# Kernel tuning notes

Measured on AMD Instinct MI355X. Metric: run time of the kernel, lower is better.

## Reference

```python
import jax, jax.numpy as jnp
import numpy as np

NUM_HEADS = 8
TEMPERATURE = 10000.0


def sine_embed(pos, dim):
    """Sine positional embedding of 2D offsets. pos [..., 2] -> [..., dim]."""
    half = dim // 2  # dims per coordinate
    dim_t = TEMPERATURE ** (2.0 * (jnp.arange(half) // 2).astype(jnp.float32) / half)
    s = pos[..., :, None] / dim_t  # [..., 2, half]
    emb = jnp.stack([jnp.sin(s[..., 0::2]), jnp.cos(s[..., 1::2])], axis=-1)
    emb = emb.reshape(s.shape[:-1] + (half,))  # interleaved sin/cos per coord
    return emb.reshape(pos.shape[:-1] + (dim,))


def setup_inputs() -> dict:
    key = jax.random.key(0)
    ks = jax.random.split(key, 16)
    N, H, W, C, K = 2, 40, 40, 256, 100
    h = NUM_HEADS
    sc = 1.0 / np.sqrt(C)
    return {
        "query_feature": jax.random.normal(ks[0], (N, H, W, C), jnp.float32),
        "query_position": jax.random.uniform(ks[1], (N, H, W, 2), jnp.float32),
        "key_feature": jax.random.normal(ks[2], (N, K, C), jnp.float32),
        "key_position": jax.random.uniform(ks[3], (N, K, 2), jnp.float32),
        # MultiheadAttention params (torch convention: weight [out, in])
        "in_proj_w": jax.random.normal(ks[4], (3 * C, C), jnp.float32) * sc,
        "in_proj_b": jnp.zeros((3 * C,), jnp.float32),
        "out_proj_w": jax.random.normal(ks[5], (C, C), jnp.float32) * sc,
        "out_proj_b": jnp.zeros((C,), jnp.float32),
        # PositionalEncodingSineLearned MLP: sine(C) -> C -> num_heads
        "pos_w1": jax.random.normal(ks[6], (C, C), jnp.float32) * sc,
        "pos_b1": jnp.zeros((C,), jnp.float32),
        "pos_w2": jax.random.normal(ks[7], (h, C), jnp.float32) * sc,
        "pos_b2": jnp.zeros((h,), jnp.float32),
        # cat_pos branch params
        "pos_trans_w": jax.random.normal(ks[8], (2, 2), jnp.float32),
        "embed_w": jax.random.normal(ks[9], (C, C + 2), jnp.float32) * 0.01,
        "embed_b": jnp.zeros((C,), jnp.float32),
    }


def reference(query_feature, query_position, key_feature, key_position,
              in_proj_w, in_proj_b, out_proj_w, out_proj_b,
              pos_w1, pos_b1, pos_w2, pos_b2,
              pos_trans_w, embed_w, embed_b):
    N, H, W, C = query_feature.shape
    h = NUM_HEADS
    d = C // h
    q = query_feature.reshape(N, -1, C)            # [N,Q,C]
    qp = query_position.reshape(N, -1, 2)          # [N,Q,2] (scale_terms = 1.0)
    Q = q.shape[1]
    K = key_feature.shape[1]

    # pairwise relative positions: [N,Q,K,2]
    rel_pos = key_position[:, None, :, :] - qp[:, :, None, :]

    # learned sine relative positional encoding -> per-head additive bias
    pe = sine_embed(rel_pos, C)                              # [N,Q,K,C]
    hid = jax.nn.relu(pe @ pos_w1.T + pos_b1)                # [N,Q,K,C]
    bias = (hid @ pos_w2.T + pos_b2).transpose(0, 3, 1, 2)   # [N,h,Q,K]

    # multihead attention with additive relative bias
    wq, wk, wv = jnp.split(in_proj_w, 3, axis=0)
    bq, bk, bv = jnp.split(in_proj_b, 3, axis=0)
    qh = ((q @ wq.T + bq).reshape(N, Q, h, d)) * (d ** -0.5)
    kh = (key_feature @ wk.T + bk).reshape(N, K, h, d)
    vh = (key_feature @ wv.T + bv).reshape(N, K, h, d)
    scores = jnp.einsum('nqhd,nkhd->nhqk', qh, kh) + bias
    attn = jax.nn.softmax(scores, axis=-1)                   # [N,h,Q,K]
    ctx = jnp.einsum('nhqk,nkhd->nqhd', attn, vh).reshape(N, Q, C)
    refined = ctx @ out_proj_w.T + out_proj_b                # [N,Q,C]

    # cat_pos: attention-weighted relative position aggregation
    attn_w = attn.mean(axis=1)                               # [N,Q,K]
    new_rel = jnp.einsum('nqk,nqkc->nqc', attn_w, jax.lax.stop_gradient(rel_pos))
    new_pos = new_rel @ pos_trans_w.T                        # [N,Q,2]

    feat = jax.nn.relu(q + refined)
    feat = jax.nn.relu(jnp.concatenate([feat, new_pos], axis=-1) @ embed_w.T + embed_b)
    return feat.reshape(N, H, W, C)
```

## Files before the change

kernel.cpp:

```cpp
#include <hip/hip_runtime.h>
#include <math.h>

typedef __bf16 bf16x8 __attribute__((ext_vector_type(8)));
typedef __bf16 bf16x4 __attribute__((ext_vector_type(4)));
typedef float  f32x4  __attribute__((ext_vector_type(4)));


#define WS_KH    0u
#define WS_VH    51200u
#define WS_EWT   102400u
#define WS_QHB   168960u
#define WS_BIASB 578560u
#define WS_KEB   2012160u
#define WS_W1B   2038560u
#define WS_W2PB  2071328u
#define WS_QEB   2073376u
#define WS_IPWT  2482976u
#define WS_OWT   2679584u

__device__ __forceinline__ float rdlane(float v, int l) {
  return __uint_as_float(__builtin_amdgcn_readlane(__float_as_uint(v), l));
}

__device__ __forceinline__ unsigned packbf(float a, float b) {
  unsigned short ua = __builtin_bit_cast(unsigned short, (__bf16)a);
  unsigned short ub = __builtin_bit_cast(unsigned short, (__bf16)b);
  return (unsigned)ua | ((unsigned)ub << 16);
}

__global__ __launch_bounds__(256, 2) void prep0_kernel(
    const float* __restrict__ ipw, const float* __restrict__ ow,
    const float* __restrict__ ew, float* __restrict__ ws)
{
  __shared__ float tile[64][65];
  int bid = blockIdx.x, t = threadIdx.x;
  int l = t & 63, gq = t >> 6;

  if (bid < 48) {
    int row0 = (bid >> 2) * 64, col0 = (bid & 3) * 64;
#pragma unroll
    for (int i = 0; i < 16; i++) {
      int r = gq * 16 + i;
      tile[r][l] = ipw[(unsigned)(row0 + r) * 256u + col0 + l];
    }
    __syncthreads();
#pragma unroll
    for (int i = 0; i < 16; i++) {
      int r = gq * 16 + i;
      ws[WS_IPWT + (unsigned)(col0 + r) * 768u + row0 + l] = tile[l][r];
    }
  } else if (bid < 64) {
    int b = bid - 48;
    int row0 = (b >> 2) * 64, col0 = (b & 3) * 64;
#pragma unroll
    for (int i = 0; i < 16; i++) {
      int r = gq * 16 + i;
      tile[r][l] = ow[(unsigned)(row0 + r) * 256u + col0 + l];
    }
    __syncthreads();
#pragma unroll
    for (int i = 0; i < 16; i++) {
      int r = gq * 16 + i;
      ws[WS_OWT + (unsigned)(col0 + r) * 256u + row0 + l] = tile[l][r];
    }
  } else {
    int b = bid - 64;
    int row0 = (b / 5) * 64, col0 = (b % 5) * 64;
#pragma unroll
    for (int i = 0; i < 16; i++) {
      int r = gq * 16 + i;
      int cin = col0 + l;
      tile[r][l] = (cin < 258) ? ew[(unsigned)(row0 + r) * 258u + cin] : 0.0f;
    }
    __syncthreads();
#pragma unroll
    for (int i = 0; i < 16; i++) {
      int r = gq * 16 + i;
      int j = col0 + r;
      if (j < 260) ws[WS_EWT + (unsigned)j * 256u + row0 + l] = tile[l][r];
    }
  }
}

__global__ __launch_bounds__(256, 2) void prep_kernel(
    const float* __restrict__ qfeat, const float* __restrict__ kfeat,
    const float* __restrict__ kpos, const float* __restrict__ qpos,
    const float* __restrict__ ipb,
    const float* __restrict__ pos_w1, const float* __restrict__ pos_w2,
    float* __restrict__ ws)
{
  __shared__ float x[8 * 256];
  int bid = blockIdx.x, t = threadIdx.x;

  if (bid < 50) {
    int r = bid * 4 + (t >> 6);
    int u = t & 63;
    float p0 = kpos[r * 2 + 0], p1 = kpos[r * 2 + 1];
    __bf16* keb = (__bf16*)(ws + WS_KEB);
    bf16x4 o;
#pragma unroll
    for (int j = 0; j < 4; j++) {
      int col = u * 4 + j;
      int c = col >> 7, i = (col & 127) >> 1;
      float p = c ? p1 : p0;
      float inv = exp2f((float)i * (-13.287712379549449f / 64.0f));
      float v = p * inv;
      o[j] = (__bf16)((col & 1) ? __cosf(v) : __sinf(v));
    }
    *(bf16x4*)(keb + r * 264 + u * 4) = o;
  } else if (bid < 114) {
    int idx = (bid - 50) * 1024 + t * 4;
    float4 v = *(const float4*)( (const float*)0 == nullptr ? nullptr : nullptr);
    (void)v;
  } else if (bid < 147) {
    return;
  } else if (bid < 547) {
    int r0 = (bid - 147) * 8;
    for (int i = t; i < 2048; i += 256) x[i] = qfeat[(unsigned)r0 * 256u + i];
    __syncthreads();
    float acc[8]; float bq = ipb[t];
#pragma unroll
    for (int rr = 0; rr < 8; rr++) acc[rr] = bq;
    const float* wqt = ws + WS_IPWT + t;
    for (int j = 0; j < 256; j += 4) {
      float w0 = wqt[(unsigned)(j + 0) * 768u];
      float w1 = wqt[(unsigned)(j + 1) * 768u];
      float w2 = wqt[(unsigned)(j + 2) * 768u];
      float w3 = wqt[(unsigned)(j + 3) * 768u];
#pragma unroll
      for (int rr = 0; rr < 8; rr++) {
        float4 x4 = *(const float4*)(x + rr * 256 + j);
        acc[rr] = fmaf(x4.x, w0, fmaf(x4.y, w1, fmaf(x4.z, w2, fmaf(x4.w, w3, acc[rr]))));
      }
    }
    __bf16* qhb = (__bf16*)(ws + WS_QHB);
#pragma unroll
    for (int rr = 0; rr < 8; rr++)
      qhb[(unsigned)(r0 + rr) * 256u + t] = (__bf16)(acc[rr] * 0.17677669529663687f);
  } else if (bid < 579) {
    int b2 = bid - 547; int n = b2 >> 4, tile = b2 & 15;
    int r0l = tile * 7; int cnt = 100 - r0l; if (cnt > 7) cnt = 7; if (cnt <= 0) return;
    int r0 = n * 100 + r0l;
    for (int i = t; i < cnt * 256; i += 256) x[i] = kfeat[(unsigned)r0 * 256u + i];
    __syncthreads();
    float ak[7], av[7]; float bk = ipb[256 + t], bv = ipb[512 + t];
#pragma unroll
    for (int rr = 0; rr < 7; rr++) { ak[rr] = bk; av[rr] = bv; }
    const float* wkt = ws + WS_IPWT + 256 + t;
    const float* wvt = ws + WS_IPWT + 512 + t;
    for (int j = 0; j < 256; j += 2) {
      float k0 = wkt[(unsigned)(j + 0) * 768u];
      float k1 = wkt[(unsigned)(j + 1) * 768u];
      float v0 = wvt[(unsigned)(j + 0) * 768u];
      float v1 = wvt[(unsigned)(j + 1) * 768u];
#pragma unroll
      for (int rr = 0; rr < 7; rr++) {
        float2 x2 = *(const float2*)(x + rr * 256 + j);
        ak[rr] = fmaf(x2.x, k0, fmaf(x2.y, k1, ak[rr]));
        av[rr] = fmaf(x2.x, v0, fmaf(x2.y, v1, av[rr]));
      }
    }
    for (int rr = 0; rr < 7; rr++) {
      if (rr < cnt) {
        ws[WS_KH + (unsigned)(r0 + rr) * 256u + t] = ak[rr];
        ws[WS_VH + (unsigned)(r0 + rr) * 256u + t] = av[rr];
      }
    }
  } else {
    int r = (bid - 579) * 4 + (t >> 6);
    int u = t & 63;
    float p0 = qpos[r * 2 + 0], p1 = qpos[r * 2 + 1];
    __bf16* qeb = (__bf16*)(ws + WS_QEB);
    bf16x4 o;
#pragma unroll
    for (int j = 0; j < 4; j++) {
      int col = u * 4 + j;
      int c = col >> 7, i = (col & 127) >> 1;
      float p = c ? p1 : p0;
      float inv = exp2f((float)i * (-13.287712379549449f / 64.0f));
      float v = p * inv;
      o[j] = (__bf16)((col & 1) ? __cosf(v) : __sinf(v));
    }
    *(bf16x4*)(qeb + r * 256 + u * 4) = o;
  }
}

__global__ __launch_bounds__(256, 2) void prep_w_kernel(
    const float* __restrict__ pos_w1, const float* __restrict__ pos_w2,
    float* __restrict__ ws)
{
  int bid = blockIdx.x, t = threadIdx.x;
  if (bid < 64) {
    int idx = bid * 1024 + t * 4;
    float4 v = *(const float4*)(pos_w1 + idx);
    bf16x4 o; o[0] = (__bf16)v.x; o[1] = (__bf16)v.y; o[2] = (__bf16)v.z; o[3] = (__bf16)v.w;
    *(bf16x4*)((__bf16*)(ws + WS_W1B) + idx) = o;
  } else {
    __bf16* w2pb = (__bf16*)(ws + WS_W2PB);
    for (int i = 0; i < 16; i++) {
      int idx = t * 16 + i;
      w2pb[idx] = (idx < 2048) ? (__bf16)pos_w2[idx] : (__bf16)0.0f;
    }
  }
}

__global__ __launch_bounds__(512, 2) void bias_kernel(
    const float* __restrict__ pos_b1, const float* __restrict__ pos_b2,
    float* __restrict__ ws)
{
  __shared__ __align__(16) char qe_smem[2][32768];
  __shared__ __align__(16) char hid_smem[2][32768];
  __shared__ __align__(16) __bf16 keb_s[256];

  int bid = blockIdx.x;
  int nk = bid / 5, g = bid - nk * 5;
  int n = nk / 100, k = nk - n * 100;
  int qbase = n * 1600 + g * 320;
  int t = threadIdx.x;
  int lane = t & 63, w = t >> 6;
  int wc = w & 3, wq = w >> 2;
  int l15 = lane & 15, quad = lane >> 4;

  const __bf16* keb = (const __bf16*)(ws + WS_KEB) + (unsigned)nk * 264u;
  const __bf16* qeb = (const __bf16*)(ws + WS_QEB);
  const __bf16* w1b = (const __bf16*)(ws + WS_W1B);
  const __bf16* w2pb = (const __bf16*)(ws + WS_W2PB);
  __bf16* biasb = (__bf16*)(ws + WS_BIASB);

  if (t < 32) *(bf16x8*)(keb_s + t * 8) = *(const bf16x8*)(keb + t * 8);

  int sr = t >> 3, ssub = t & 7, sswz = (sr & 7) << 4;
  {
    const __bf16* src = qeb + (unsigned)(qbase + sr) * 256u + ssub * 32;
    char* dst = qe_smem[0] + sr * 512;
#pragma unroll
    for (int u = 0; u < 4; u++) {
      bf16x8 v = *(const bf16x8*)(src + u * 8);
      *(bf16x8*)(dst + ((ssub * 64 + u * 16) ^ sswz)) = v;
    }
  }

  int xm = (l15 & 7) << 4;
  int colx[8];
#pragma unroll
  for (int kc = 0; kc < 8; kc++) colx[kc] = ((kc * 64 + quad * 16) ^ xm);
  const __bf16* w1p = w1b + (unsigned)(wc * 64 + l15) * 256u + quad * 8;

  float b1a[4][4];
#pragma unroll
  for (int ct = 0; ct < 4; ct++)
#pragma unroll
    for (int r = 0; r < 4; r++) b1a[ct][r] = pos_b1[wc * 64 + ct * 16 + quad * 4 + r];
  float b2v[4];
#pragma unroll
  for (int r = 0; r < 4; r++) b2v[r] = pos_b2[(quad * 4 + r) & 7];

  f32x4 zero4; zero4[0] = 0.f; zero4[1] = 0.f; zero4[2] = 0.f; zero4[3] = 0.f;

  __syncthreads();

  bf16x8 af[8][4];
#pragma unroll
  for (int kc = 0; kc < 8; kc++) {
    bf16x8 ke8 = *(const bf16x8*)(keb_s + kc * 32 + quad * 8);
#pragma unroll
    for (int ct = 0; ct < 4; ct++) {
      bf16x8 w8 = *(const bf16x8*)(w1p + ct * 4096 + kc * 32);
      bf16x8 a;
#pragma unroll
      for (int p2 = 0; p2 < 4; p2++) {
        float we = (float)w8[2 * p2], wo = (float)w8[2 * p2 + 1];
        float sk = (float)ke8[2 * p2], ck = (float)ke8[2 * p2 + 1];
        a[2 * p2]     = (__bf16)fmaf(wo, sk, -(we * ck));
        a[2 * p2 + 1] = (__bf16)fmaf(we, sk, wo * ck);
      }
      af[kc][ct] = a;
    }
  }

  unsigned long long bias_pk[5];

  auto gemm2 = [&](int tg) {
    bf16x8 w2f[8];
#pragma unroll
    for (int kc = 0; kc < 8; kc++)
      w2f[kc] = *(const bf16x8*)(w2pb + (unsigned)l15 * 256u + kc * 32 + quad * 8);
    int row = wc * 16 + l15;
    const char* hbase = hid_smem[tg & 1] + row * 512;
    int hxm = (l15 & 7) << 4;
    f32x4 acc2 = zero4;
#pragma unroll
    for (int kc = 0; kc < 8; kc++) {
      bf16x8 hf = *(const bf16x8*)(hbase + ((kc * 64 + quad * 16) ^ hxm));
      acc2 = __builtin_amdgcn_mfma_f32_16x16x32_bf16(w2f[kc], hf, acc2, 0, 0, 0);
    }
    unsigned lo = packbf(acc2[0] + b2v[0], acc2[1] + b2v[1]);
    unsigned hi = packbf(acc2[2] + b2v[2], acc2[3] + b2v[3]);
    return (unsigned long long)lo | ((unsigned long long)hi << 32);
  };

#pragma unroll
  for (int tt = 0; tt < 5; tt++) {
    bf16x8 qv[4];
    if (tt < 4) {
      const __bf16* src = qeb + (unsigned)(qbase + (tt + 1) * 64 + sr) * 256u + ssub * 32;
#pragma unroll
      for (int u = 0; u < 4; u++) qv[u] = *(const bf16x8*)(src + u * 8);
    }

    if (tt > 0 && wq == 0) bias_pk[tt - 1] = gemm2(tt - 1);

    f32x4 acc[4][2];
#pragma unroll
    for (int ct = 0; ct < 4; ct++)
#pragma unroll
      for (int nt = 0; nt < 2; nt++) acc[ct][nt] = zero4;

#pragma unroll
    for (int kc = 0; kc < 8; kc++) {
#pragma unroll
      for (int nt = 0; nt < 2; nt++) {
        int row = wq * 32 + nt * 16 + l15;
        bf16x8 qf = *(const bf16x8*)(qe_smem[tt & 1] + row * 512 + colx[kc]);
        acc[0][nt] = __builtin_amdgcn_mfma_f32_16x16x32_bf16(af[kc][0], qf, acc[0][nt], 0, 0, 0);
        acc[1][nt] = __builtin_amdgcn_mfma_f32_16x16x32_bf16(af[kc][1], qf, acc[1][nt], 0, 0, 0);
        acc[2][nt] = __builtin_amdgcn_mfma_f32_16x16x32_bf16(af[kc][2], qf, acc[2][nt], 0, 0, 0);
        acc[3][nt] = __builtin_amdgcn_mfma_f32_16x16x32_bf16(af[kc][3], qf, acc[3][nt], 0, 0, 0);
      }
    }

#pragma unroll
    for (int ct = 0; ct < 4; ct++) {
#pragma unroll
      for (int nt = 0; nt < 2; nt++) {
        int q = wq * 32 + nt * 16 + l15;
        unsigned lo = packbf(fmaxf(acc[ct][nt][0] + b1a[ct][0], 0.f),
                             fmaxf(acc[ct][nt][1] + b1a[ct][1], 0.f));
        unsigned hi = packbf(fmaxf(acc[ct][nt][2] + b1a[ct][2], 0.f),
                             fmaxf(acc[ct][nt][3] + b1a[ct][3], 0.f));
        int cbyte = wc * 128 + ct * 32 + quad * 8;
        char* p = hid_smem[tt & 1] + q * 512 + (cbyte ^ ((q & 7) << 4));
        *(unsigned long long*)p = (unsigned long long)lo | ((unsigned long long)hi << 32);
      }
    }

    if (tt < 4) {
      char* dst = qe_smem[(tt + 1) & 1] + sr * 512;
#pragma unroll
      for (int u = 0; u < 4; u++)
        *(bf16x8*)(dst + ((ssub * 64 + u * 16) ^ sswz)) = qv[u];
    }

    __syncthreads();
  }

  if (wq == 0) {
    bias_pk[4] = gemm2(4);
    if (quad < 2) {
      int row = wc * 16 + l15;
#pragma unroll
      for (int tg = 0; tg < 5; tg++) {
        int qg = qbase + tg * 64 + row;
        *(unsigned long long*)(biasb + (unsigned)qg * 896u + (unsigned)k * 8u + quad * 4)
            = bias_pk[tg];
      }
    }
  }
}

__global__ __launch_bounds__(256, 4) void attn_kernel(
    const float* __restrict__ qfeat, const float* __restrict__ qpos,
    const float* __restrict__ kpos,
    const float* __restrict__ out_b,
    const float* __restrict__ embed_b, const float* __restrict__ ptw,
    const float* __restrict__ ws, float* __restrict__ out)
{
  __shared__ float qh_s[4 * 8 * 36];
  __shared__ float attn_s[4 * 8 * 116];
  __shared__ float ctx_s[4 * 264];
  __shared__ float cat_s[4 * 264];
  __shared__ float aw_s[4 * 104];

  int bid = blockIdx.x;
  int qg0 = bid * 4;
  int n = bid / 400;
  int t = threadIdx.x;

  const __bf16* qhb = (const __bf16*)(ws + WS_QHB);
  const __bf16* biasb = (const __bf16*)(ws + WS_BIASB);
  const float* kh = ws + WS_KH;
  const float* vh = ws + WS_VH;

  for (int i = t; i < 1024; i += 256) {
    int q = i >> 8, c = i & 255;
    qh_s[(q * 8 + (c >> 5)) * 36 + (c & 31)] = (float)qhb[(unsigned)(qg0 + q) * 256u + c];
  }
  __syncthreads();

  for (int i = 0; i < 4; i++) {
    int p = t + i * 256;
    if (p < 800) {
      int k = p >> 3, h = p & 7;
      const float4* kf = (const float4*)(kh + (unsigned)(n * 100 + k) * 256u + h * 32);
      float4 kv[8];
#pragma unroll
      for (int dd = 0; dd < 8; dd++) kv[dd] = kf[dd];
#pragma unroll
      for (int q = 0; q < 4; q++) {
        const float4* qf = (const float4*)(qh_s + (q * 8 + h) * 36);
        float s = (float)biasb[((unsigned)(qg0 + q) * 112u + k) * 8u + h];
#pragma unroll
        for (int dd = 0; dd < 8; dd++) {
          float4 qv = qf[dd];
          s += kv[dd].x * qv.x + kv[dd].y * qv.y + kv[dd].z * qv.z + kv[dd].w * qv.w;
        }
        attn_s[(q * 8 + h) * 116 + k] = s;
      }
    }
  }
  __syncthreads();

  {
    int q = t >> 6, h = (t >> 3) & 7, j = t & 7;
    float* row = attn_s + (q * 8 + h) * 116;
    float mx = -1e30f;
    for (int k = j; k < 100; k += 8) mx = fmaxf(mx, row[k]);
    mx = fmaxf(mx, __shfl_xor(mx, 1, 8));
    mx = fmaxf(mx, __shfl_xor(mx, 2, 8));
    mx = fmaxf(mx, __shfl_xor(mx, 4, 8));
    float sum = 0.f;
    for (int k = j; k < 100; k += 8) { float e = __expf(row[k] - mx); row[k] = e; sum += e; }
    sum += __shfl_xor(sum, 1, 8);
    sum += __shfl_xor(sum, 2, 8);
    sum += __shfl_xor(sum, 4, 8);
    float inv = 1.0f / sum;
    for (int k = j; k < 100; k += 8) row[k] *= inv;
  }
  __syncthreads();

  for (int p = t; p < 416; p += 256) {
    int q = p / 104, k = p % 104;
    if (k < 100) {
      float s = 0.f;
#pragma unroll
      for (int h = 0; h < 8; h++) s += attn_s[(q * 8 + h) * 116 + k];
      aw_s[q * 104 + k] = s * 0.125f;
    }
  }
  {
    int c = t, h = c >> 5;
    float a0 = 0.f, a1 = 0.f, a2 = 0.f, a3 = 0.f;
    const float* vp = vh + (unsigned)(n * 100) * 256u + c;
    const float* r0 = attn_s + (0 * 8 + h) * 116;
    const float* r1 = attn_s + (1 * 8 + h) * 116;
    const float* r2 = attn_s + (2 * 8 + h) * 116;
    const float* r3 = attn_s + (3 * 8 + h) * 116;
#pragma unroll 4
    for (int k = 0; k < 100; k++) {
      float vv = vp[(unsigned)k * 256u];
      a0 = fmaf(r0[k], vv, a0);
      a1 = fmaf(r1[k], vv, a1);
      a2 = fmaf(r2[k], vv, a2);
      a3 = fmaf(r3[k], vv, a3);
    }
    ctx_s[0 * 264 + c] = a0; ctx_s[1 * 264 + c] = a1;
    ctx_s[2 * 264 + c] = a2; ctx_s[3 * 264 + c] = a3;
  }
  __syncthreads();

  if (t < 8) {
    int q = t >> 1, cd = t & 1;
    float qp = qpos[(qg0 + q) * 2 + cd];
    float s = 0.f;
    for (int k = 0; k < 100; k++)
      s = fmaf(aw_s[q * 104 + k], kpos[(n * 100 + k) * 2 + cd] - qp, s);
    float so = __shfl_xor(s, 1, 2);
    if (cd == 0) cat_s[q * 264 + 256] = ptw[0] * s + ptw[1] * so;
    else         cat_s[q * 264 + 257] = ptw[2] * so + ptw[3] * s;
  }

  {
    int c = t, lane = t & 63;
    float ob = out_b[c];
    float acc0 = ob, acc1 = ob, acc2 = ob, acc3 = ob;
    const float* wcol = ws + WS_OWT + c;
    for (int ch = 0; ch < 4; ch++) {
      float v0 = ctx_s[0 * 264 + ch * 64 + lane];
      float v1 = ctx_s[1 * 264 + ch * 64 + lane];
      float v2 = ctx_s[2 * 264 + ch * 64 + lane];
      float v3 = ctx_s[3 * 264 + ch * 64 + lane];
#pragma unroll 4
      for (int j4 = 0; j4 < 16; j4++) {
        int jg = ch * 64 + j4 * 4;
        float w0 = wcol[(unsigned)(jg + 0) * 256u];
        float w1 = wcol[(unsigned)(jg + 1) * 256u];
        float w2 = wcol[(unsigned)(jg + 2) * 256u];
        float w3 = wcol[(unsigned)(jg + 3) * 256u];
        int jb = j4 * 4;
        acc0 = fmaf(rdlane(v0, jb + 0), w0, acc0);
        acc1 = fmaf(rdlane(v1, jb + 0), w0, acc1);
        acc2 = fmaf(rdlane(v2, jb + 0), w0, acc2);
        acc3 = fmaf(rdlane(v3, jb + 0), w0, acc3);
        acc0 = fmaf(rdlane(v0, jb + 1), w1, acc0);
        acc1 = fmaf(rdlane(v1, jb + 1), w1, acc1);
        acc2 = fmaf(rdlane(v2, jb + 1), w1, acc2);
        acc3 = fmaf(rdlane(v3, jb + 1), w1, acc3);
        acc0 = fmaf(rdlane(v0, jb + 2), w2, acc0);
        acc1 = fmaf(rdlane(v1, jb + 2), w2, acc1);
        acc2 = fmaf(rdlane(v2, jb + 2), w2, acc2);
        acc3 = fmaf(rdlane(v3, jb + 2), w2, acc3);
        acc0 = fmaf(rdlane(v0, jb + 3), w3, acc0);
        acc1 = fmaf(rdlane(v1, jb + 3), w3, acc1);
        acc2 = fmaf(rdlane(v2, jb + 3), w3, acc2);
        acc3 = fmaf(rdlane(v3, jb + 3), w3, acc3);
      }
    }
    cat_s[0 * 264 + c] = fmaxf(qfeat[(unsigned)(qg0 + 0) * 256u + c] + acc0, 0.f);
    cat_s[1 * 264 + c] = fmaxf(qfeat[(unsigned)(qg0 + 1) * 256u + c] + acc1, 0.f);
    cat_s[2 * 264 + c] = fmaxf(qfeat[(unsigned)(qg0 + 2) * 256u + c] + acc2, 0.f);
    cat_s[3 * 264 + c] = fmaxf(qfeat[(unsigned)(qg0 + 3) * 256u + c] + acc3, 0.f);
  }
  __syncthreads();

  {
    int c = t, lane = t & 63;
    float eb = embed_b[c];
    float acc0 = eb, acc1 = eb, acc2 = eb, acc3 = eb;
    const float* ecol = ws + WS_EWT + c;
    for (int ch = 0; ch < 4; ch++) {
      float v0 = cat_s[0 * 264 + ch * 64 + lane];
      float v1 = cat_s[1 * 264 + ch * 64 + lane];
      float v2 = cat_s[2 * 264 + ch * 64 + lane];
      float v3 = cat_s[3 * 264 + ch * 64 + lane];
#pragma unroll 4
      for (int j4 = 0; j4 < 16; j4++) {
        int jg = ch * 64 + j4 * 4;
        float w0 = ecol[(unsigned)(jg + 0) * 256u];
        float w1 = ecol[(unsigned)(jg + 1) * 256u];
        float w2 = ecol[(unsigned)(jg + 2) * 256u];
        float w3 = ecol[(unsigned)(jg + 3) * 256u];
        int jb = j4 * 4;
        acc0 = fmaf(rdlane(v0, jb + 0), w0, acc0);
        acc1 = fmaf(rdlane(v1, jb + 0), w0, acc1);
        acc2 = fmaf(rdlane(v2, jb + 0), w0, acc2);
        acc3 = fmaf(rdlane(v3, jb + 0), w0, acc3);
        acc0 = fmaf(rdlane(v0, jb + 1), w1, acc0);
        acc1 = fmaf(rdlane(v1, jb + 1), w1, acc1);
        acc2 = fmaf(rdlane(v2, jb + 1), w1, acc2);
        acc3 = fmaf(rdlane(v3, jb + 1), w1, acc3);
        acc0 = fmaf(rdlane(v0, jb + 2), w2, acc0);
        acc1 = fmaf(rdlane(v1, jb + 2), w2, acc1);
        acc2 = fmaf(rdlane(v2, jb + 2), w2, acc2);
        acc3 = fmaf(rdlane(v3, jb + 2), w2, acc3);
        acc0 = fmaf(rdlane(v0, jb + 3), w3, acc0);
        acc1 = fmaf(rdlane(v1, jb + 3), w3, acc1);
        acc2 = fmaf(rdlane(v2, jb + 3), w3, acc2);
        acc3 = fmaf(rdlane(v3, jb + 3), w3, acc3);
      }
    }
    float wtx = ecol[256u * 256u];
    float wty = ecol[257u * 256u];
    acc0 += cat_s[0 * 264 + 256] * wtx + cat_s[0 * 264 + 257] * wty;
    acc1 += cat_s[1 * 264 + 256] * wtx + cat_s[1 * 264 + 257] * wty;
    acc2 += cat_s[2 * 264 + 256] * wtx + cat_s[2 * 264 + 257] * wty;
    acc3 += cat_s[3 * 264 + 256] * wtx + cat_s[3 * 264 + 257] * wty;
    out[(unsigned)(qg0 + 0) * 256u + c] = fmaxf(acc0, 0.f);
    out[(unsigned)(qg0 + 1) * 256u + c] = fmaxf(acc1, 0.f);
    out[(unsigned)(qg0 + 2) * 256u + c] = fmaxf(acc2, 0.f);
    out[(unsigned)(qg0 + 3) * 256u + c] = fmaxf(acc3, 0.f);
  }
}

extern "C" void kernel_launch(void* const* d_in, const int* in_sizes, int n_in,
                              void* d_out, int out_size, void* d_ws, size_t ws_size,
                              hipStream_t stream)
{
  const float* query_feature  = (const float*)d_in[0];
  const float* query_position = (const float*)d_in[1];
  const float* key_feature    = (const float*)d_in[2];
  const float* key_position   = (const float*)d_in[3];
  const float* in_proj_w      = (const float*)d_in[4];
  const float* in_proj_b      = (const float*)d_in[5];
  const float* out_proj_w     = (const float*)d_in[6];
  const float* out_proj_b     = (const float*)d_in[7];
  const float* pos_w1         = (const float*)d_in[8];
  const float* pos_b1         = (const float*)d_in[9];
  const float* pos_w2         = (const float*)d_in[10];
  const float* pos_b2         = (const float*)d_in[11];
  const float* pos_trans_w    = (const float*)d_in[12];
  const float* embed_w        = (const float*)d_in[13];
  const float* embed_b        = (const float*)d_in[14];
  float* ws  = (float*)d_ws;
  float* out = (float*)d_out;

  hipLaunchKernelGGL(prep0_kernel, dim3(84), dim3(256), 0, stream,
                     in_proj_w, out_proj_w, embed_w, ws);
  hipLaunchKernelGGL(prep_w_kernel, dim3(65), dim3(256), 0, stream,
                     pos_w1, pos_w2, ws);
  hipLaunchKernelGGL(prep_kernel, dim3(1379), dim3(256), 0, stream,
                     query_feature, key_feature, key_position, query_position,
                     in_proj_b, pos_w1, pos_w2, ws);
  hipLaunchKernelGGL(bias_kernel, dim3(1000), dim3(512), 0, stream,
                     pos_b1, pos_b2, ws);
  hipLaunchKernelGGL(attn_kernel, dim3(800), dim3(256), 0, stream,
                     query_feature, query_position, key_position,
                     out_proj_b, embed_b, pos_trans_w,
                     ws, out);
}
```

Baseline: 282.2 us.

## Merge prep kernels, drop in_proj transpose, retile bias kernel for occupancy

Folds the separate weight-transpose and weight-conversion kernels into the main prep kernel, cutting two launches. The Q/K/V projections now read in_proj_w rows directly with float4 loads, so the transposed copy of that matrix is no longer built. The bias MLP kernel is retiled to 32-query tiles per step over 8 channel-sliced waves. This halves its shared memory, allows 4 blocks per CU, doubles the grid, and stores the second GEMM's results immediately instead of buffering them. The cost is that per-thread row reads of the weights are strided across lanes, and the second GEMM reloads its weights every step.

```diff
diff --git a/kernel.cpp b/kernel.cpp
--- a/kernel.cpp
+++ b/kernel.cpp
@@ -15,8 +15,7 @@
 #define WS_W1B   2038560u
 #define WS_W2PB  2071328u
 #define WS_QEB   2073376u
-#define WS_IPWT  2482976u
-#define WS_OWT   2679584u
+#define WS_OWT   2482976u
 
 __device__ __forceinline__ float rdlane(float v, int l) {
   return __uint_as_float(__builtin_amdgcn_readlane(__float_as_uint(v), l));
@@ -28,65 +27,12 @@
   return (unsigned)ua | ((unsigned)ub << 16);
 }
 
-__global__ __launch_bounds__(256, 2) void prep0_kernel(
-    const float* __restrict__ ipw, const float* __restrict__ ow,
-    const float* __restrict__ ew, float* __restrict__ ws)
-{
-  __shared__ float tile[64][65];
-  int bid = blockIdx.x, t = threadIdx.x;
-  int l = t & 63, gq = t >> 6;
-
-  if (bid < 48) {
-    int row0 = (bid >> 2) * 64, col0 = (bid & 3) * 64;
-#pragma unroll
-    for (int i = 0; i < 16; i++) {
-      int r = gq * 16 + i;
-      tile[r][l] = ipw[(unsigned)(row0 + r) * 256u + col0 + l];
-    }
-    __syncthreads();
-#pragma unroll
-    for (int i = 0; i < 16; i++) {
-      int r = gq * 16 + i;
-      ws[WS_IPWT + (unsigned)(col0 + r) * 768u + row0 + l] = tile[l][r];
-    }
-  } else if (bid < 64) {
-    int b = bid - 48;
-    int row0 = (b >> 2) * 64, col0 = (b & 3) * 64;
-#pragma unroll
-    for (int i = 0; i < 16; i++) {
-      int r = gq * 16 + i;
-      tile[r][l] = ow[(unsigned)(row0 + r) * 256u + col0 + l];
-    }
-    __syncthreads();
-#pragma unroll
-    for (int i = 0; i < 16; i++) {
-      int r = gq * 16 + i;
-      ws[WS_OWT + (unsigned)(col0 + r) * 256u + row0 + l] = tile[l][r];
-    }
-  } else {
-    int b = bid - 64;
-    int row0 = (b / 5) * 64, col0 = (b % 5) * 64;
-#pragma unroll
-    for (int i = 0; i < 16; i++) {
-      int r = gq * 16 + i;
-      int cin = col0 + l;
-      tile[r][l] = (cin < 258) ? ew[(unsigned)(row0 + r) * 258u + cin] : 0.0f;
-    }
-    __syncthreads();
-#pragma unroll
-    for (int i = 0; i < 16; i++) {
-      int r = gq * 16 + i;
-      int j = col0 + r;
-      if (j < 260) ws[WS_EWT + (unsigned)j * 256u + row0 + l] = tile[l][r];
-    }
-  }
-}
-
 __global__ __launch_bounds__(256, 2) void prep_kernel(
     const float* __restrict__ qfeat, const float* __restrict__ kfeat,
     const float* __restrict__ kpos, const float* __restrict__ qpos,
-    const float* __restrict__ ipb,
+    const float* __restrict__ ipw, const float* __restrict__ ipb,
     const float* __restrict__ pos_w1, const float* __restrict__ pos_w2,
+    const float* __restrict__ ow, const float* __restrict__ ew,
     float* __restrict__ ws)
 {
   __shared__ float x[8 * 256];
@@ -110,8 +56,15 @@
     *(bf16x4*)(keb + r * 264 + u * 4) = o;
   } else if (bid < 114) {
     int idx = (bid - 50) * 1024 + t * 4;
-    float4 v = *(const float4*)( (const float*)0 == nullptr ? nullptr : nullptr);
-    (void)v;
+    float4 v = *(const float4*)(pos_w1 + idx);
+    bf16x4 o; o[0] = (__bf16)v.x; o[1] = (__bf16)v.y; o[2] = (__bf16)v.z; o[3] = (__bf16)v.w;
+    *(bf16x4*)((__bf16*)(ws + WS_W1B) + idx) = o;
+  } else if (bid == 114) {
+    __bf16* w2pb = (__bf16*)(ws + WS_W2PB);
+    for (int i = 0; i < 16; i++) {
+      int idx = t * 16 + i;
+      w2pb[idx] = (idx < 2048) ? (__bf16)pos_w2[idx] : (__bf16)0.0f;
+    }
   } else if (bid < 147) {
     return;
   } else if (bid < 547) {
@@ -121,16 +74,13 @@
     float acc[8]; float bq = ipb[t];
 #pragma unroll
     for (int rr = 0; rr < 8; rr++) acc[rr] = bq;
-    const float* wqt = ws + WS_IPWT + t;
+    const float* wrow = ipw + (unsigned)t * 256u;
     for (int j = 0; j < 256; j += 4) {
-      float w0 = wqt[(unsigned)(j + 0) * 768u];
-      float w1 = wqt[(unsigned)(j + 1) * 768u];
-      float w2 = wqt[(unsigned)(j + 2) * 768u];
-      float w3 = wqt[(unsigned)(j + 3) * 768u];
+      float4 w4 = *(const float4*)(wrow + j);
 #pragma unroll
       for (int rr = 0; rr < 8; rr++) {
         float4 x4 = *(const float4*)(x + rr * 256 + j);
-        acc[rr] = fmaf(x4.x, w0, fmaf(x4.y, w1, fmaf(x4.z, w2, fmaf(x4.w, w3, acc[rr]))));
+        acc[rr] = fmaf(x4.x, w4.x, fmaf(x4.y, w4.y, fmaf(x4.z, w4.z, fmaf(x4.w, w4.w, acc[rr]))));
       }
     }
     __bf16* qhb = (__bf16*)(ws + WS_QHB);
@@ -146,18 +96,16 @@
     float ak[7], av[7]; float bk = ipb[256 + t], bv = ipb[512 + t];
 #pragma unroll
     for (int rr = 0; rr < 7; rr++) { ak[rr] = bk; av[rr] = bv; }
-    const float* wkt = ws + WS_IPWT + 256 + t;
-    const float* wvt = ws + WS_IPWT + 512 + t;
-    for (int j = 0; j < 256; j += 2) {
-      float k0 = wkt[(unsigned)(j + 0) * 768u];
-      float k1 = wkt[(unsigned)(j + 1) * 768u];
-      float v0 = wvt[(unsigned)(j + 0) * 768u];
-      float v1 = wvt[(unsigned)(j + 1) * 768u];
+    const float* wkr = ipw + (unsigned)(256 + t) * 256u;
+    const float* wvr = ipw + (unsigned)(512 + t) * 256u;
+    for (int j = 0; j < 256; j += 4) {
+      float4 wk4 = *(const float4*)(wkr + j);
+      float4 wv4 = *(const float4*)(wvr + j);
 #pragma unroll
       for (int rr = 0; rr < 7; rr++) {
-        float2 x2 = *(const float2*)(x + rr * 256 + j);
-        ak[rr] = fmaf(x2.x, k0, fmaf(x2.y, k1, ak[rr]));
-        av[rr] = fmaf(x2.x, v0, fmaf(x2.y, v1, av[rr]));
+        float4 x4 = *(const float4*)(x + rr * 256 + j);
+        ak[rr] = fmaf(x4.x, wk4.x, fmaf(x4.y, wk4.y, fmaf(x4.z, wk4.z, fmaf(x4.w, wk4.w, ak[rr]))));
+        av[rr] = fmaf(x4.x, wv4.x, fmaf(x4.y, wv4.y, fmaf(x4.z, wv4.z, fmaf(x4.w, wv4.w, av[rr]))));
       }
     }
     for (int rr = 0; rr < 7; rr++) {
@@ -166,7 +114,7 @@
         ws[WS_VH + (unsigned)(r0 + rr) * 256u + t] = av[rr];
       }
     }
-  } else {
+  } else if (bid < 1379) {
     int r = (bid - 579) * 4 + (t >> 6);
     int u = t & 63;
     float p0 = qpos[r * 2 + 0], p1 = qpos[r * 2 + 1];
@@ -182,43 +130,57 @@
       o[j] = (__bf16)((col & 1) ? __cosf(v) : __sinf(v));
     }
     *(bf16x4*)(qeb + r * 256 + u * 4) = o;
+  } else if (bid < 1395) {
+    __shared__ float tile[64][65];
+    int b = bid - 1379;
+    int row0 = (b >> 2) * 64, col0 = (b & 3) * 64;
+    int l = t & 63, gq = t >> 6;
+#pragma unroll
+    for (int i = 0; i < 16; i++) {
+      int r = gq * 16 + i;
+      tile[r][l] = ow[(unsigned)(row0 + r) * 256u + col0 + l];
+    }
+    __syncthreads();
+#pragma unroll
+    for (int i = 0; i < 16; i++) {
+      int r = gq * 16 + i;
+      ws[WS_OWT + (unsigned)(col0 + r) * 256u + row0 + l] = tile[l][r];
+    }
+  } else {
+    __shared__ float tile[64][65];
+    int b = bid - 1395;
+    int row0 = (b / 5) * 64, col0 = (b % 5) * 64;
+    int l = t & 63, gq = t >> 6;
+#pragma unroll
+    for (int i = 0; i < 16; i++) {
+      int r = gq * 16 + i;
+      int cin = col0 + l;
+      tile[r][l] = (cin < 258) ? ew[(unsigned)(row0 + r) * 258u + cin] : 0.0f;
+    }
+    __syncthreads();
+#pragma unroll
+    for (int i = 0; i < 16; i++) {
+      int r = gq * 16 + i;
+      int j = col0 + r;
+      if (j < 260) ws[WS_EWT + (unsigned)j * 256u + row0 + l] = tile[l][r];
+    }
   }
 }
 
-__global__ __launch_bounds__(256, 2) void prep_w_kernel(
-    const float* __restrict__ pos_w1, const float* __restrict__ pos_w2,
-    float* __restrict__ ws)
-{
-  int bid = blockIdx.x, t = threadIdx.x;
-  if (bid < 64) {
-    int idx = bid * 1024 + t * 4;
-    float4 v = *(const float4*)(pos_w1 + idx);
-    bf16x4 o; o[0] = (__bf16)v.x; o[1] = (__bf16)v.y; o[2] = (__bf16)v.z; o[3] = (__bf16)v.w;
-    *(bf16x4*)((__bf16*)(ws + WS_W1B) + idx) = o;
-  } else {
-    __bf16* w2pb = (__bf16*)(ws + WS_W2PB);
-    for (int i = 0; i < 16; i++) {
-      int idx = t * 16 + i;
-      w2pb[idx] = (idx < 2048) ? (__bf16)pos_w2[idx] : (__bf16)0.0f;
-    }
-  }
-}
-
-__global__ __launch_bounds__(512, 2) void bias_kernel(
+__global__ __launch_bounds__(512, 4) void bias_kernel(
     const float* __restrict__ pos_b1, const float* __restrict__ pos_b2,
     float* __restrict__ ws)
 {
-  __shared__ __align__(16) char qe_smem[2][32768];
-  __shared__ __align__(16) char hid_smem[2][32768];
+  __shared__ __align__(16) char qe_smem[2][16384];
+  __shared__ __align__(16) char hid_smem[2][16384];
   __shared__ __align__(16) __bf16 keb_s[256];
 
   int bid = blockIdx.x;
-  int nk = bid / 5, g = bid - nk * 5;
+  int nk = bid / 10, g = bid - nk * 10;
   int n = nk / 100, k = nk - n * 100;
-  int qbase = n * 1600 + g * 320;
+  int qbase = n * 1600 + g * 160;
   int t = threadIdx.x;
-  int lane = t & 63, w = t >> 6;
-  int wc = w & 3, wq = w >> 2;
+  int lane = t & 63, wc = t >> 6;
   int l15 = lane & 15, quad = lane >> 4;
 
   const __bf16* keb = (const __bf16*)(ws + WS_KEB) + (unsigned)nk * 264u;
@@ -229,42 +191,36 @@
 
   if (t < 32) *(bf16x8*)(keb_s + t * 8) = *(const bf16x8*)(keb + t * 8);
 
-  int sr = t >> 3, ssub = t & 7, sswz = (sr & 7) << 4;
+  int sr = t >> 4, ssub = t & 15, sswz = (sr & 7) << 4;
   {
-    const __bf16* src = qeb + (unsigned)(qbase + sr) * 256u + ssub * 32;
+    const __bf16* src = qeb + (unsigned)(qbase + sr) * 256u + ssub * 16;
     char* dst = qe_smem[0] + sr * 512;
 #pragma unroll
-    for (int u = 0; u < 4; u++) {
+    for (int u = 0; u < 2; u++) {
       bf16x8 v = *(const bf16x8*)(src + u * 8);
-      *(bf16x8*)(dst + ((ssub * 64 + u * 16) ^ sswz)) = v;
+      *(bf16x8*)(dst + ((ssub * 32 + u * 16) ^ sswz)) = v;
     }
   }
 
   int xm = (l15 & 7) << 4;
-  int colx[8];
-#pragma unroll
-  for (int kc = 0; kc < 8; kc++) colx[kc] = ((kc * 64 + quad * 16) ^ xm);
-  const __bf16* w1p = w1b + (unsigned)(wc * 64 + l15) * 256u + quad * 8;
-
-  float b1a[4][4];
-#pragma unroll
-  for (int ct = 0; ct < 4; ct++)
-#pragma unroll
-    for (int r = 0; r < 4; r++) b1a[ct][r] = pos_b1[wc * 64 + ct * 16 + quad * 4 + r];
-  float b2v[4];
-#pragma unroll
-  for (int r = 0; r < 4; r++) b2v[r] = pos_b2[(quad * 4 + r) & 7];
+  const __bf16* w1p = w1b + (unsigned)(wc * 32 + l15) * 256u + quad * 8;
+
+  float b1a[2][4];
+#pragma unroll
+  for (int ct = 0; ct < 2; ct++)
+#pragma unroll
+    for (int r = 0; r < 4; r++) b1a[ct][r] = pos_b1[wc * 32 + ct * 16 + quad * 4 + r];
 
   f32x4 zero4; zero4[0] = 0.f; zero4[1] = 0.f; zero4[2] = 0.f; zero4[3] = 0.f;
 
   __syncthreads();
 
-  bf16x8 af[8][4];
+  bf16x8 af[8][2];
 #pragma unroll
   for (int kc = 0; kc < 8; kc++) {
     bf16x8 ke8 = *(const bf16x8*)(keb_s + kc * 32 + quad * 8);
 #pragma unroll
-    for (int ct = 0; ct < 4; ct++) {
+    for (int ct = 0; ct < 2; ct++) {
       bf16x8 w8 = *(const bf16x8*)(w1p + ct * 4096 + kc * 32);
       bf16x8 a;
 #pragma unroll
@@ -278,41 +234,40 @@
     }
   }
 
-  unsigned long long bias_pk[5];
-
-  auto gemm2 = [&](int tg) {
-    bf16x8 w2f[8];
-#pragma unroll
-    for (int kc = 0; kc < 8; kc++)
-      w2f[kc] = *(const bf16x8*)(w2pb + (unsigned)l15 * 256u + kc * 32 + quad * 8);
+  auto gemm2_store = [&](int tg) {
     int row = wc * 16 + l15;
     const char* hbase = hid_smem[tg & 1] + row * 512;
     int hxm = (l15 & 7) << 4;
     f32x4 acc2 = zero4;
 #pragma unroll
     for (int kc = 0; kc < 8; kc++) {
+      bf16x8 w2f = *(const bf16x8*)(w2pb + (unsigned)l15 * 256u + kc * 32 + quad * 8);
       bf16x8 hf = *(const bf16x8*)(hbase + ((kc * 64 + quad * 16) ^ hxm));
-      acc2 = __builtin_amdgcn_mfma_f32_16x16x32_bf16(w2f[kc], hf, acc2, 0, 0, 0);
-    }
-    unsigned lo = packbf(acc2[0] + b2v[0], acc2[1] + b2v[1]);
-    unsigned hi = packbf(acc2[2] + b2v[2], acc2[3] + b2v[3]);
-    return (unsigned long long)lo | ((unsigned long long)hi << 32);
+      acc2 = __builtin_amdgcn_mfma_f32_16x16x32_bf16(w2f, hf, acc2, 0, 0, 0);
+    }
+    if (quad < 2) {
+      int qg = qbase + tg * 32 + row;
+      bf16x4 o;
+#pragma unroll
+      for (int r = 0; r < 4; r++) o[r] = (__bf16)(acc2[r] + pos_b2[quad * 4 + r]);
+      *(bf16x4*)(biasb + (unsigned)qg * 896u + (unsigned)k * 8u + quad * 4) = o;
+    }
   };
 
 #pragma unroll
   for (int tt = 0; tt < 5; tt++) {
-    bf16x8 qv[4];
+    bf16x8 qv[2];
     if (tt < 4) {
-      const __bf16* src = qeb + (unsigned)(qbase + (tt + 1) * 64 + sr) * 256u + ssub * 32;
-#pragma unroll
-      for (int u = 0; u < 4; u++) qv[u] = *(const bf16x8*)(src + u * 8);
-    }
-
-    if (tt > 0 && wq == 0) bias_pk[tt - 1] = gemm2(tt - 1);
-
-    f32x4 acc[4][2];
-#pragma unroll
-    for (int ct = 0; ct < 4; ct++)
+      const __bf16* src = qeb + (unsigned)(qbase + (tt + 1) * 32 + sr) * 256u + ssub * 16;
+#pragma unroll
+      for (int u = 0; u < 2; u++) qv[u] = *(const bf16x8*)(src + u * 8);
+    }
+
+    if (tt > 0 && wc < 2) gemm2_store(tt - 1);
+
+    f32x4 acc[2][2];
+#pragma unroll
+    for (int ct = 0; ct < 2; ct++)
 #pragma unroll
       for (int nt = 0; nt < 2; nt++) acc[ct][nt] = zero4;
 
@@ -320,25 +275,23 @@
     for (int kc = 0; kc < 8; kc++) {
 #pragma unroll
       for (int nt = 0; nt < 2; nt++) {
-        int row = wq * 32 + nt * 16 + l15;
-        bf16x8 qf = *(const bf16x8*)(qe_smem[tt & 1] + row * 512 + colx[kc]);
+        int row = nt * 16 + l15;
+        bf16x8 qf = *(const bf16x8*)(qe_smem[tt & 1] + row * 512 + ((kc * 64 + quad * 16) ^ xm));
         acc[0][nt] = __builtin_amdgcn_mfma_f32_16x16x32_bf16(af[kc][0], qf, acc[0][nt], 0, 0, 0);
         acc[1][nt] = __builtin_amdgcn_mfma_f32_16x16x32_bf16(af[kc][1], qf, acc[1][nt], 0, 0, 0);
-        acc[2][nt] = __builtin_amdgcn_mfma_f32_16x16x32_bf16(af[kc][2], qf, acc[2][nt], 0, 0, 0);
-        acc[3][nt] = __builtin_amdgcn_mfma_f32_16x16x32_bf16(af[kc][3], qf, acc[3][nt], 0, 0, 0);
-      }
-    }
-
-#pragma unroll
-    for (int ct = 0; ct < 4; ct++) {
+      }
+    }
+
+#pragma unroll
+    for (int ct = 0; ct < 2; ct++) {
 #pragma unroll
       for (int nt = 0; nt < 2; nt++) {
-        int q = wq * 32 + nt * 16 + l15;
+        int q = nt * 16 + l15;
         unsigned lo = packbf(fmaxf(acc[ct][nt][0] + b1a[ct][0], 0.f),
                              fmaxf(acc[ct][nt][1] + b1a[ct][1], 0.f));
         unsigned hi = packbf(fmaxf(acc[ct][nt][2] + b1a[ct][2], 0.f),
                              fmaxf(acc[ct][nt][3] + b1a[ct][3], 0.f));
-        int cbyte = wc * 128 + ct * 32 + quad * 8;
+        int cbyte = wc * 64 + ct * 32 + quad * 8;
         char* p = hid_smem[tt & 1] + q * 512 + (cbyte ^ ((q & 7) << 4));
         *(unsigned long long*)p = (unsigned long long)lo | ((unsigned long long)hi << 32);
       }
@@ -347,25 +300,14 @@
     if (tt < 4) {
       char* dst = qe_smem[(tt + 1) & 1] + sr * 512;
 #pragma unroll
-      for (int u = 0; u < 4; u++)
-        *(bf16x8*)(dst + ((ssub * 64 + u * 16) ^ sswz)) = qv[u];
+      for (int u = 0; u < 2; u++)
+        *(bf16x8*)(dst + ((ssub * 32 + u * 16) ^ sswz)) = qv[u];
     }
 
     __syncthreads();
   }
 
-  if (wq == 0) {
-    bias_pk[4] = gemm2(4);
-    if (quad < 2) {
-      int row = wc * 16 + l15;
-#pragma unroll
-      for (int tg = 0; tg < 5; tg++) {
-        int qg = qbase + tg * 64 + row;
-        *(unsigned long long*)(biasb + (unsigned)qg * 896u + (unsigned)k * 8u + quad * 4)
-            = bias_pk[tg];
-      }
-    }
-  }
+  if (wc < 2) gemm2_store(4);
 }
 
 __global__ __launch_bounds__(256, 4) void attn_kernel(
@@ -593,14 +535,11 @@
   float* ws  = (float*)d_ws;
   float* out = (float*)d_out;
 
-  hipLaunchKernelGGL(prep0_kernel, dim3(84), dim3(256), 0, stream,
-                     in_proj_w, out_proj_w, embed_w, ws);
-  hipLaunchKernelGGL(prep_w_kernel, dim3(65), dim3(256), 0, stream,
-                     pos_w1, pos_w2, ws);
-  hipLaunchKernelGGL(prep_kernel, dim3(1379), dim3(256), 0, stream,
+  hipLaunchKernelGGL(prep_kernel, dim3(1415), dim3(256), 0, stream,
                      query_feature, key_feature, key_position, query_position,
-                     in_proj_b, pos_w1, pos_w2, ws);
-  hipLaunchKernelGGL(bias_kernel, dim3(1000), dim3(512), 0, stream,
+                     in_proj_w, in_proj_b, pos_w1, pos_w2,
+                     out_proj_w, embed_w, ws);
+  hipLaunchKernelGGL(bias_kernel, dim3(2000), dim3(512), 0, stream,
                      pos_b1, pos_b2, ws);
   hipLaunchKernelGGL(attn_kernel, dim3(800), dim3(256), 0, stream,
                      query_feature, query_position, key_position,
```

Measured after the change: 276.6 us. 2.0% less time.

## Merge weight-prep kernels into prep kernel and read untransposed in_proj weights directly

Applied to the files above, without the earlier changes.

Folds the two weight-preparation launches (transposes and bf16 conversions) into the main prep kernel as extra block ranges, removing two kernel launches and their serialization. The Q/K/V projections now read rows of the original in_proj weight with float4 loads instead of a transposed workspace copy, which eliminates the in_proj transpose. The trade-off is that each thread now reads a distinct weight row, so loads are strided across lanes rather than coalesced, which may cost memory efficiency in the projection blocks.

```diff
diff --git a/kernel.cpp b/kernel.cpp
--- a/kernel.cpp
+++ b/kernel.cpp
@@ -15,8 +15,7 @@
 #define WS_W1B   2038560u
 #define WS_W2PB  2071328u
 #define WS_QEB   2073376u
-#define WS_IPWT  2482976u
-#define WS_OWT   2679584u
+#define WS_OWT   2482976u
 
 __device__ __forceinline__ float rdlane(float v, int l) {
   return __uint_as_float(__builtin_amdgcn_readlane(__float_as_uint(v), l));
@@ -28,65 +27,12 @@
   return (unsigned)ua | ((unsigned)ub << 16);
 }
 
-__global__ __launch_bounds__(256, 2) void prep0_kernel(
-    const float* __restrict__ ipw, const float* __restrict__ ow,
-    const float* __restrict__ ew, float* __restrict__ ws)
-{
-  __shared__ float tile[64][65];
-  int bid = blockIdx.x, t = threadIdx.x;
-  int l = t & 63, gq = t >> 6;
-
-  if (bid < 48) {
-    int row0 = (bid >> 2) * 64, col0 = (bid & 3) * 64;
-#pragma unroll
-    for (int i = 0; i < 16; i++) {
-      int r = gq * 16 + i;
-      tile[r][l] = ipw[(unsigned)(row0 + r) * 256u + col0 + l];
-    }
-    __syncthreads();
-#pragma unroll
-    for (int i = 0; i < 16; i++) {
-      int r = gq * 16 + i;
-      ws[WS_IPWT + (unsigned)(col0 + r) * 768u + row0 + l] = tile[l][r];
-    }
-  } else if (bid < 64) {
-    int b = bid - 48;
-    int row0 = (b >> 2) * 64, col0 = (b & 3) * 64;
-#pragma unroll
-    for (int i = 0; i < 16; i++) {
-      int r = gq * 16 + i;
-      tile[r][l] = ow[(unsigned)(row0 + r) * 256u + col0 + l];
-    }
-    __syncthreads();
-#pragma unroll
-    for (int i = 0; i < 16; i++) {
-      int r = gq * 16 + i;
-      ws[WS_OWT + (unsigned)(col0 + r) * 256u + row0 + l] = tile[l][r];
-    }
-  } else {
-    int b = bid - 64;
-    int row0 = (b / 5) * 64, col0 = (b % 5) * 64;
-#pragma unroll
-    for (int i = 0; i < 16; i++) {
-      int r = gq * 16 + i;
-      int cin = col0 + l;
-      tile[r][l] = (cin < 258) ? ew[(unsigned)(row0 + r) * 258u + cin] : 0.0f;
-    }
-    __syncthreads();
-#pragma unroll
-    for (int i = 0; i < 16; i++) {
-      int r = gq * 16 + i;
-      int j = col0 + r;
-      if (j < 260) ws[WS_EWT + (unsigned)j * 256u + row0 + l] = tile[l][r];
-    }
-  }
-}
-
 __global__ __launch_bounds__(256, 2) void prep_kernel(
     const float* __restrict__ qfeat, const float* __restrict__ kfeat,
     const float* __restrict__ kpos, const float* __restrict__ qpos,
-    const float* __restrict__ ipb,
+    const float* __restrict__ ipw, const float* __restrict__ ipb,
     const float* __restrict__ pos_w1, const float* __restrict__ pos_w2,
+    const float* __restrict__ ow, const float* __restrict__ ew,
     float* __restrict__ ws)
 {
   __shared__ float x[8 * 256];
@@ -110,8 +56,15 @@
     *(bf16x4*)(keb + r * 264 + u * 4) = o;
   } else if (bid < 114) {
     int idx = (bid - 50) * 1024 + t * 4;
-    float4 v = *(const float4*)( (const float*)0 == nullptr ? nullptr : nullptr);
-    (void)v;
+    float4 v = *(const float4*)(pos_w1 + idx);
+    bf16x4 o; o[0] = (__bf16)v.x; o[1] = (__bf16)v.y; o[2] = (__bf16)v.z; o[3] = (__bf16)v.w;
+    *(bf16x4*)((__bf16*)(ws + WS_W1B) + idx) = o;
+  } else if (bid == 114) {
+    __bf16* w2pb = (__bf16*)(ws + WS_W2PB);
+    for (int i = 0; i < 16; i++) {
+      int idx = t * 16 + i;
+      w2pb[idx] = (idx < 2048) ? (__bf16)pos_w2[idx] : (__bf16)0.0f;
+    }
   } else if (bid < 147) {
     return;
   } else if (bid < 547) {
@@ -121,16 +74,13 @@
     float acc[8]; float bq = ipb[t];
 #pragma unroll
     for (int rr = 0; rr < 8; rr++) acc[rr] = bq;
-    const float* wqt = ws + WS_IPWT + t;
+    const float* wrow = ipw + (unsigned)t * 256u;
     for (int j = 0; j < 256; j += 4) {
-      float w0 = wqt[(unsigned)(j + 0) * 768u];
-      float w1 = wqt[(unsigned)(j + 1) * 768u];
-      float w2 = wqt[(unsigned)(j + 2) * 768u];
-      float w3 = wqt[(unsigned)(j + 3) * 768u];
+      float4 w4 = *(const float4*)(wrow + j);
 #pragma unroll
       for (int rr = 0; rr < 8; rr++) {
         float4 x4 = *(const float4*)(x + rr * 256 + j);
-        acc[rr] = fmaf(x4.x, w0, fmaf(x4.y, w1, fmaf(x4.z, w2, fmaf(x4.w, w3, acc[rr]))));
+        acc[rr] = fmaf(x4.x, w4.x, fmaf(x4.y, w4.y, fmaf(x4.z, w4.z, fmaf(x4.w, w4.w, acc[rr]))));
       }
     }
     __bf16* qhb = (__bf16*)(ws + WS_QHB);
@@ -146,18 +96,16 @@
     float ak[7], av[7]; float bk = ipb[256 + t], bv = ipb[512 + t];
 #pragma unroll
     for (int rr = 0; rr < 7; rr++) { ak[rr] = bk; av[rr] = bv; }
-    const float* wkt = ws + WS_IPWT + 256 + t;
-    const float* wvt = ws + WS_IPWT + 512 + t;
-    for (int j = 0; j < 256; j += 2) {
-      float k0 = wkt[(unsigned)(j + 0) * 768u];
-      float k1 = wkt[(unsigned)(j + 1) * 768u];
-      float v0 = wvt[(unsigned)(j + 0) * 768u];
-      float v1 = wvt[(unsigned)(j + 1) * 768u];
+    const float* wkr = ipw + (unsigned)(256 + t) * 256u;
+    const float* wvr = ipw + (unsigned)(512 + t) * 256u;
+    for (int j = 0; j < 256; j += 4) {
+      float4 wk4 = *(const float4*)(wkr + j);
+      float4 wv4 = *(const float4*)(wvr + j);
 #pragma unroll
       for (int rr = 0; rr < 7; rr++) {
-        float2 x2 = *(const float2*)(x + rr * 256 + j);
-        ak[rr] = fmaf(x2.x, k0, fmaf(x2.y, k1, ak[rr]));
-        av[rr] = fmaf(x2.x, v0, fmaf(x2.y, v1, av[rr]));
+        float4 x4 = *(const float4*)(x + rr * 256 + j);
+        ak[rr] = fmaf(x4.x, wk4.x, fmaf(x4.y, wk4.y, fmaf(x4.z, wk4.z, fmaf(x4.w, wk4.w, ak[rr]))));
+        av[rr] = fmaf(x4.x, wv4.x, fmaf(x4.y, wv4.y, fmaf(x4.z, wv4.z, fmaf(x4.w, wv4.w, av[rr]))));
       }
     }
     for (int rr = 0; rr < 7; rr++) {
@@ -166,7 +114,7 @@
         ws[WS_VH + (unsigned)(r0 + rr) * 256u + t] = av[rr];
       }
     }
-  } else {
+  } else if (bid < 1379) {
     int r = (bid - 579) * 4 + (t >> 6);
     int u = t & 63;
     float p0 = qpos[r * 2 + 0], p1 = qpos[r * 2 + 1];
@@ -182,24 +130,39 @@
       o[j] = (__bf16)((col & 1) ? __cosf(v) : __sinf(v));
     }
     *(bf16x4*)(qeb + r * 256 + u * 4) = o;
-  }
-}
-
-__global__ __launch_bounds__(256, 2) void prep_w_kernel(
-    const float* __restrict__ pos_w1, const float* __restrict__ pos_w2,
-    float* __restrict__ ws)
-{
-  int bid = blockIdx.x, t = threadIdx.x;
-  if (bid < 64) {
-    int idx = bid * 1024 + t * 4;
-    float4 v = *(const float4*)(pos_w1 + idx);
-    bf16x4 o; o[0] = (__bf16)v.x; o[1] = (__bf16)v.y; o[2] = (__bf16)v.z; o[3] = (__bf16)v.w;
-    *(bf16x4*)((__bf16*)(ws + WS_W1B) + idx) = o;
+  } else if (bid < 1395) {
+    __shared__ float tile[64][65];
+    int b = bid - 1379;
+    int row0 = (b >> 2) * 64, col0 = (b & 3) * 64;
+    int l = t & 63, gq = t >> 6;
+#pragma unroll
+    for (int i = 0; i < 16; i++) {
+      int r = gq * 16 + i;
+      tile[r][l] = ow[(unsigned)(row0 + r) * 256u + col0 + l];
+    }
+    __syncthreads();
+#pragma unroll
+    for (int i = 0; i < 16; i++) {
+      int r = gq * 16 + i;
+      ws[WS_OWT + (unsigned)(col0 + r) * 256u + row0 + l] = tile[l][r];
+    }
   } else {
-    __bf16* w2pb = (__bf16*)(ws + WS_W2PB);
+    __shared__ float tile[64][65];
+    int b = bid - 1395;
+    int row0 = (b / 5) * 64, col0 = (b % 5) * 64;
+    int l = t & 63, gq = t >> 6;
+#pragma unroll
     for (int i = 0; i < 16; i++) {
-      int idx = t * 16 + i;
-      w2pb[idx] = (idx < 2048) ? (__bf16)pos_w2[idx] : (__bf16)0.0f;
+      int r = gq * 16 + i;
+      int cin = col0 + l;
+      tile[r][l] = (cin < 258) ? ew[(unsigned)(row0 + r) * 258u + cin] : 0.0f;
+    }
+    __syncthreads();
+#pragma unroll
+    for (int i = 0; i < 16; i++) {
+      int r = gq * 16 + i;
+      int j = col0 + r;
+      if (j < 260) ws[WS_EWT + (unsigned)j * 256u + row0 + l] = tile[l][r];
     }
   }
 }
@@ -593,13 +556,10 @@
   float* ws  = (float*)d_ws;
   float* out = (float*)d_out;
 
-  hipLaunchKernelGGL(prep0_kernel, dim3(84), dim3(256), 0, stream,
-                     in_proj_w, out_proj_w, embed_w, ws);
-  hipLaunchKernelGGL(prep_w_kernel, dim3(65), dim3(256), 0, stream,
-                     pos_w1, pos_w2, ws);
-  hipLaunchKernelGGL(prep_kernel, dim3(1379), dim3(256), 0, stream,
+  hipLaunchKernelGGL(prep_kernel, dim3(1415), dim3(256), 0, stream,
                      query_feature, key_feature, key_position, query_position,
-                     in_proj_b, pos_w1, pos_w2, ws);
+                     in_proj_w, in_proj_b, pos_w1, pos_w2,
+                     out_proj_w, embed_w, ws);
   hipLaunchKernelGGL(bias_kernel, dim3(1000), dim3(512), 0, stream,
                      pos_b1, pos_b2, ws);
   hipLaunchKernelGGL(attn_kernel, dim3(800), dim3(256), 0, stream,
```

Result: faster. 267.1 us (-5.3%).
